# Kernel tuning notes

Measured on AMD Instinct MI355X. Metric: run time of the kernel, lower is better.

The kernel has to match this reference:

```python
import jax, jax.numpy as jnp
import numpy as np

N_NODES = 100000
N_EDGES = 1600000
D = 64


def setup_inputs() -> dict:
    key = jax.random.key(0)
    ks = jax.random.split(key, 8)
    x = jax.random.normal(ks[0], (N_NODES, D), dtype=jnp.float32)
    edge_index = jax.random.randint(ks[1], (2, N_EDGES), 0, N_NODES, dtype=jnp.int64)
    scale = 1.0 / np.sqrt(D)
    W1 = jax.random.normal(ks[2], (D, D), dtype=jnp.float32) * scale
    W2 = jax.random.normal(ks[3], (D, D), dtype=jnp.float32) * scale
    W3 = jax.random.normal(ks[4], (D, D), dtype=jnp.float32) * scale
    b1 = jnp.zeros((D,), dtype=jnp.float32)
    b2 = jnp.zeros((D,), dtype=jnp.float32)
    b3 = jnp.zeros((D,), dtype=jnp.float32)
    return {"x": x, "edge_index": edge_index, "W1": W1, "b1": b1,
            "W2": W2, "b2": b2, "W3": W3, "b3": b3}


def reference(x, edge_index, W1, b1, W2, b2, W3, b3):
    # 3-layer GCN (PyG GCNConv semantics): add self-loops, symmetric
    # degree normalization, linear transform, scatter-add aggregation.
    # Dropout is identity at inference.
    N = x.shape[0]
    loops = jnp.arange(N, dtype=edge_index.dtype)
    src = jnp.concatenate([edge_index[0], loops])  # [E+N]
    dst = jnp.concatenate([edge_index[1], loops])  # [E+N]
    # degree of each node (in-degree at dst, self-loops included)
    deg = jax.ops.segment_sum(jnp.ones(src.shape[0], dtype=x.dtype), dst,
                              num_segments=N)
    dis = jnp.where(deg > 0, jax.lax.rsqrt(jnp.maximum(deg, 1.0)), 0.0)
    norm = dis[src] * dis[dst]  # [E+N]

    def gcn_layer(h, W, b):
        h = h @ W                                   # [N, d_out]
        msg = norm[:, None] * h[src]                # gather + scale, [E+N, d_out]
        agg = jax.ops.segment_sum(msg, dst, num_segments=N)  # scatter-add
        return agg + b

    h = jax.nn.relu(gcn_layer(x, W1, b1))
    h = jax.nn.relu(gcn_layer(h, W2, b2))
    return gcn_layer(h, W3, b3)
```

## Files before the change

kernel.cpp:

```cpp
#include <hip/hip_runtime.h>

#define NN 100000
#define NE 1600000

typedef __attribute__((ext_vector_type(16))) int i32x16;

#define NBKT 196
#define NBLK 128
#define EPB  (NE / NBLK)
#define PTH  512

__global__ __launch_bounds__(PTH) void k_pcount(const int* __restrict__ dst,
                                                int* __restrict__ pcount) {
  __shared__ int lcnt[NBKT];
  int t = threadIdx.x, b = blockIdx.x;
  for (int i = t; i < NBKT; i += PTH) lcnt[i] = 0;
  __syncthreads();
  int base = b * EPB;
  for (int i = t; i < EPB; i += PTH)
    atomicAdd(&lcnt[dst[base + i] >> 9], 1);
  __syncthreads();
  for (int i = t; i < NBKT; i += PTH)
    pcount[i * NBLK + b] = lcnt[i];
}

__global__ __launch_bounds__(1024) void k_pscan(int* __restrict__ pcount) {
  __shared__ int sh[1024];
  const int TOT = NBKT * NBLK;
  int t = threadIdx.x;
  int base = t * 25;
  int v[25];
  int s = 0;
  #pragma unroll
  for (int k = 0; k < 25; ++k) {
    v[k] = (base + k < TOT) ? pcount[base + k] : 0;
    s += v[k];
  }
  sh[t] = s;
  __syncthreads();
  for (int off = 1; off < 1024; off <<= 1) {
    int x = (t >= off) ? sh[t - off] : 0;
    __syncthreads();
    sh[t] += x;
    __syncthreads();
  }
  int ex = sh[t] - s;
  #pragma unroll
  for (int k = 0; k < 25; ++k) {
    if (base + k < TOT) pcount[base + k] = ex;
    ex += v[k];
  }
}

__global__ __launch_bounds__(PTH) void k_pscatter(const int* __restrict__ src,
                                                  const int* __restrict__ dst,
                                                  const int* __restrict__ pcount,
                                                  int* __restrict__ staged) {
  __shared__ int lpos[NBKT];
  int t = threadIdx.x, b = blockIdx.x;
  for (int i = t; i < NBKT; i += PTH) lpos[i] = pcount[i * NBLK + b];
  __syncthreads();
  int base = b * EPB;
  for (int i = t; i < EPB; i += PTH) {
    int s = src[base + i], d = dst[base + i];
    int pos = atomicAdd(&lpos[d >> 9], 1);
    staged[pos] = s | ((d & 511) << 17);
  }
}

__global__ __launch_bounds__(PTH) void k_bucket(const int* __restrict__ staged,
                                                const int* __restrict__ pcount,
                                                int* __restrict__ rowptr,
                                                float* __restrict__ dis,
                                                int* __restrict__ col) {
  __shared__ int lcnt[PTH];
  __shared__ int lscan[PTH];
  __shared__ int lpos[PTH];
  int t = threadIdx.x, bkt = blockIdx.x;
  int sbeg = pcount[bkt * NBLK];
  int send = (bkt == NBKT - 1) ? NE : pcount[(bkt + 1) * NBLK];

  lcnt[t] = 0;
  __syncthreads();
  for (int i = sbeg + t; i < send; i += PTH)
    atomicAdd(&lcnt[(unsigned)staged[i] >> 17], 1);
  __syncthreads();

  int v = lcnt[t];
  lscan[t] = v;
  __syncthreads();
  for (int off = 1; off < PTH; off <<= 1) {
    int x = (t >= off) ? lscan[t - off] : 0;
    __syncthreads();
    lscan[t] += x;
    __syncthreads();
  }
  int gbase = sbeg + lscan[t] - v;
  int node = bkt * 512 + t;
  if (node < NN) {
    rowptr[node] = gbase;
    dis[node] = rsqrtf((float)(v + 1));
  }
  lpos[t] = gbase;
  if (bkt == NBKT - 1 && t == 0) rowptr[NN] = NE;
  __syncthreads();

  for (int i = sbeg + t; i < send; i += PTH) {
    int e = staged[i];
    col[atomicAdd(&lpos[(unsigned)e >> 17], 1)] = e & 0x1FFFF;
  }
}

__device__ __forceinline__ unsigned bf16rne(float x) {
  unsigned u = __float_as_uint(x);
  return (u + 0x7fffu + ((u >> 16) & 1u)) >> 16;
}

__global__ __launch_bounds__(256) void k_xform(const float* __restrict__ h,
                                               const float* __restrict__ W,
                                               const float* __restrict__ dis,
                                               unsigned short* __restrict__ ts) {
  __shared__ float hT[64][132];
  __shared__ float Wl[64][68];
  const int tid = threadIdx.x;
  const int R0 = blockIdx.x * 128;

  {
    const float4* W4 = (const float4*)W;
    #pragma unroll
    for (int j = 0; j < 4; ++j) {
      int idx = tid + 256 * j;
      float4 v = W4[idx];
      int k = idx >> 4;
      int c = (idx & 15) * 4;
      Wl[k][c + 0] = v.x; Wl[k][c + 1] = v.y;
      Wl[k][c + 2] = v.z; Wl[k][c + 3] = v.w;
    }
  }
  {
    #pragma unroll
    for (int j = 0; j < 8; ++j) {
      int idx = tid + 256 * j;
      int r = idx >> 4;
      int k = (idx & 15) * 4;
      int rg = R0 + r; if (rg > NN - 1) rg = NN - 1;
      float4 v = *(const float4*)(h + (size_t)rg * 64 + k);
      hT[k + 0][r] = v.x; hT[k + 1][r] = v.y;
      hT[k + 2][r] = v.z; hT[k + 3][r] = v.w;
    }
  }
  __syncthreads();

  const int tx = tid & 7;
  const int ty = tid >> 3;
  float acc[4][8];
  #pragma unroll
  for (int i = 0; i < 4; ++i)
    #pragma unroll
    for (int j = 0; j < 8; ++j) acc[i][j] = 0.f;

  #pragma unroll 4
  for (int k = 0; k < 64; ++k) {
    float4 hv = *(const float4*)&hT[k][ty * 4];
    float4 w0 = *(const float4*)&Wl[k][tx * 8];
    float4 w1 = *(const float4*)&Wl[k][tx * 8 + 4];
    float hh[4] = {hv.x, hv.y, hv.z, hv.w};
    float wc[8] = {w0.x, w0.y, w0.z, w0.w, w1.x, w1.y, w1.z, w1.w};
    #pragma unroll
    for (int i = 0; i < 4; ++i)
      #pragma unroll
      for (int j = 0; j < 8; ++j)
        acc[i][j] = fmaf(hh[i], wc[j], acc[i][j]);
  }

  #pragma unroll
  for (int i = 0; i < 4; ++i) {
    int r = R0 + ty * 4 + i;
    if (r < NN) {
      float dr = dis[r];
      uint4 pk;
      pk.x = bf16rne(acc[i][0] * dr) | (bf16rne(acc[i][1] * dr) << 16);
      pk.y = bf16rne(acc[i][2] * dr) | (bf16rne(acc[i][3] * dr) << 16);
      pk.z = bf16rne(acc[i][4] * dr) | (bf16rne(acc[i][5] * dr) << 16);
      pk.w = bf16rne(acc[i][6] * dr) | (bf16rne(acc[i][7] * dr) << 16);
      *(uint4*)(ts + (size_t)r * 64 + tx * 8) = pk;
    }
  }
}

__global__ __launch_bounds__(256) void k_fuse(
    const unsigned short* __restrict__ ts, const int* __restrict__ rowptr,
    const int* __restrict__ col, const float* __restrict__ dis,
    const float* __restrict__ bias, const float* __restrict__ Wn,
    unsigned short* __restrict__ tnext)
{
  __shared__ float Wl[64][68];
  __shared__ float hh[32][68];
  const int tid  = threadIdx.x;
  const int lane = tid & 63;
  const int slot = lane >> 4;
  const int fq   = lane & 15;
  const int R0   = blockIdx.x * 32;
  const int wloc = tid >> 6;
  const int wid  = __builtin_amdgcn_readfirstlane(
                     (int)(blockIdx.x * 4 + wloc));
  const int n0   = wid * 8;

  {
    const float4* W4 = (const float4*)Wn;
    #pragma unroll
    for (int j = 0; j < 4; ++j) {
      int idx = tid + 256 * j;
      float4 v = W4[idx];
      int k = idx >> 4;
      int c = (idx & 15) * 4;
      Wl[k][c + 0] = v.x; Wl[k][c + 1] = v.y;
      Wl[k][c + 2] = v.z; Wl[k][c + 3] = v.w;
    }
  }

  const float4 bv = *(const float4*)(bias + fq * 4);
  const float m_self = (slot == 0) ? 1.f : 0.f;

  i32x16 rp;
  asm volatile("s_load_dwordx16 %0, %1, 0x0\n\ts_waitcnt lgkmcnt(0)"
               : "=s"(rp) : "s"(rowptr + n0));

  float a[8][4];
  #pragma unroll
  for (int i = 0; i < 8; ++i) {
    const uint2 sv = *(const uint2*)(ts + (size_t)(n0 + i) * 64 + fq * 4);
    a[i][0] = m_self * __uint_as_float(sv.x << 16);
    a[i][1] = m_self * __uint_as_float(sv.x & 0xffff0000u);
    a[i][2] = m_self * __uint_as_float(sv.y << 16);
    a[i][3] = m_self * __uint_as_float(sv.y & 0xffff0000u);
  }

  #pragma unroll
  for (int i = 0; i < 8; ++i) {
    const int r0 = rp[i], r1 = rp[i + 1];
    #pragma unroll
    for (int s = 0; s < 4; ++s) {
      int e = r0 + s * 4 + slot;
      int c = col[e];
      bool valid = e < r1;
      c = valid ? c : 0;
      float m = valid ? 1.f : 0.f;
      const uint2 gv = *(const uint2*)(ts + (size_t)c * 64 + fq * 4);
      a[i][0] = fmaf(m, __uint_as_float(gv.x << 16),         a[i][0]);
      a[i][1] = fmaf(m, __uint_as_float(gv.x & 0xffff0000u), a[i][1]);
      a[i][2] = fmaf(m, __uint_as_float(gv.y << 16),         a[i][2]);
      a[i][3] = fmaf(m, __uint_as_float(gv.y & 0xffff0000u), a[i][3]);
    }
  }

  #pragma unroll
  for (int i = 0; i < 8; ++i) {
    const int r1 = rp[i + 1];
    #pragma unroll 1
    for (int e0 = rp[i] + 16; e0 < r1; e0 += 8) {
      #pragma unroll
      for (int s = 0; s < 2; ++s) {
        int e = e0 + s * 4 + slot;
        int c = col[e];
        bool valid = e < r1;
        c = valid ? c : 0;
        float m = valid ? 1.f : 0.f;
        const uint2 gv = *(const uint2*)(ts + (size_t)c * 64 + fq * 4);
        a[i][0] = fmaf(m, __uint_as_float(gv.x << 16),         a[i][0]);
        a[i][1] = fmaf(m, __uint_as_float(gv.x & 0xffff0000u), a[i][1]);
        a[i][2] = fmaf(m, __uint_as_float(gv.y << 16),         a[i][2]);
        a[i][3] = fmaf(m, __uint_as_float(gv.y & 0xffff0000u), a[i][3]);
      }
    }
  }

  #pragma unroll
  for (int i = 0; i < 8; ++i) {
    const int node = n0 + i;
    const float dn = dis[node];
    float s0 = a[i][0], s1 = a[i][1], s2 = a[i][2], s3 = a[i][3];
    s0 += __shfl_xor(s0, 16); s1 += __shfl_xor(s1, 16);
    s2 += __shfl_xor(s2, 16); s3 += __shfl_xor(s3, 16);
    s0 += __shfl_xor(s0, 32); s1 += __shfl_xor(s1, 32);
    s2 += __shfl_xor(s2, 32); s3 += __shfl_xor(s3, 32);
    float4 o;
    o.x = fmaxf(fmaf(dn, s0, bv.x), 0.f);
    o.y = fmaxf(fmaf(dn, s1, bv.y), 0.f);
    o.z = fmaxf(fmaf(dn, s2, bv.z), 0.f);
    o.w = fmaxf(fmaf(dn, s3, bv.w), 0.f);
    if (lane < 16)
      *(float4*)&hh[wloc * 8 + i][fq * 4] = o;
  }
  __syncthreads();

  const int tx = tid & 7;
  const int ty = tid >> 3;
  float acc[8];
  #pragma unroll
  for (int j = 0; j < 8; ++j) acc[j] = 0.f;
  #pragma unroll 4
  for (int k = 0; k < 64; ++k) {
    float hkv = hh[ty][k];
    float4 w0 = *(const float4*)&Wl[k][tx * 8];
    float4 w1 = *(const float4*)&Wl[k][tx * 8 + 4];
    acc[0] = fmaf(hkv, w0.x, acc[0]); acc[1] = fmaf(hkv, w0.y, acc[1]);
    acc[2] = fmaf(hkv, w0.z, acc[2]); acc[3] = fmaf(hkv, w0.w, acc[3]);
    acc[4] = fmaf(hkv, w1.x, acc[4]); acc[5] = fmaf(hkv, w1.y, acc[5]);
    acc[6] = fmaf(hkv, w1.z, acc[6]); acc[7] = fmaf(hkv, w1.w, acc[7]);
  }
  {
    int r = R0 + ty;
    float dr = dis[r];
    uint4 pk;
    pk.x = bf16rne(acc[0] * dr) | (bf16rne(acc[1] * dr) << 16);
    pk.y = bf16rne(acc[2] * dr) | (bf16rne(acc[3] * dr) << 16);
    pk.z = bf16rne(acc[4] * dr) | (bf16rne(acc[5] * dr) << 16);
    pk.w = bf16rne(acc[6] * dr) | (bf16rne(acc[7] * dr) << 16);
    *(uint4*)(tnext + (size_t)r * 64 + tx * 8) = pk;
  }
}

__global__ __launch_bounds__(256) void k_agg(
    const unsigned short* __restrict__ ts, const int* __restrict__ rowptr,
    const int* __restrict__ col, const float* __restrict__ dis,
    const float* __restrict__ bias, float* __restrict__ out)
{
  const int lane = threadIdx.x & 63;
  const int slot = lane >> 4;
  const int fq   = lane & 15;
  const int wid  = __builtin_amdgcn_readfirstlane(
                     (int)((blockIdx.x * blockDim.x + threadIdx.x) >> 6));
  const int n0   = wid * 8;
  if (n0 >= NN) return;

  const float4 bv = *(const float4*)(bias + fq * 4);
  const float m_self = (slot == 0) ? 1.f : 0.f;

  i32x16 rp;
  asm volatile("s_load_dwordx16 %0, %1, 0x0\n\ts_waitcnt lgkmcnt(0)"
               : "=s"(rp) : "s"(rowptr + n0));

  float a[8][4];
  #pragma unroll
  for (int i = 0; i < 8; ++i) {
    const uint2 sv = *(const uint2*)(ts + (size_t)(n0 + i) * 64 + fq * 4);
    a[i][0] = m_self * __uint_as_float(sv.x << 16);
    a[i][1] = m_self * __uint_as_float(sv.x & 0xffff0000u);
    a[i][2] = m_self * __uint_as_float(sv.y << 16);
    a[i][3] = m_self * __uint_as_float(sv.y & 0xffff0000u);
  }

  #pragma unroll
  for (int i = 0; i < 8; ++i) {
    const int r0 = rp[i], r1 = rp[i + 1];
    #pragma unroll
    for (int s = 0; s < 4; ++s) {
      int e = r0 + s * 4 + slot;
      int c = col[e];
      bool valid = e < r1;
      c = valid ? c : 0;
      float m = valid ? 1.f : 0.f;
      const uint2 gv = *(const uint2*)(ts + (size_t)c * 64 + fq * 4);
      a[i][0] = fmaf(m, __uint_as_float(gv.x << 16),         a[i][0]);
      a[i][1] = fmaf(m, __uint_as_float(gv.x & 0xffff0000u), a[i][1]);
      a[i][2] = fmaf(m, __uint_as_float(gv.y << 16),         a[i][2]);
      a[i][3] = fmaf(m, __uint_as_float(gv.y & 0xffff0000u), a[i][3]);
    }
  }

  #pragma unroll
  for (int i = 0; i < 8; ++i) {
    const int r1 = rp[i + 1];
    #pragma unroll 1
    for (int e0 = rp[i] + 16; e0 < r1; e0 += 8) {
      #pragma unroll
      for (int s = 0; s < 2; ++s) {
        int e = e0 + s * 4 + slot;
        int c = col[e];
        bool valid = e < r1;
        c = valid ? c : 0;
        float m = valid ? 1.f : 0.f;
        const uint2 gv = *(const uint2*)(ts + (size_t)c * 64 + fq * 4);
        a[i][0] = fmaf(m, __uint_as_float(gv.x << 16),         a[i][0]);
        a[i][1] = fmaf(m, __uint_as_float(gv.x & 0xffff0000u), a[i][1]);
        a[i][2] = fmaf(m, __uint_as_float(gv.y << 16),         a[i][2]);
        a[i][3] = fmaf(m, __uint_as_float(gv.y & 0xffff0000u), a[i][3]);
      }
    }
  }

  #pragma unroll
  for (int i = 0; i < 8; ++i) {
    const int node = n0 + i;
    const float dn = dis[node];
    float s0 = a[i][0], s1 = a[i][1], s2 = a[i][2], s3 = a[i][3];
    s0 += __shfl_xor(s0, 16); s1 += __shfl_xor(s1, 16);
    s2 += __shfl_xor(s2, 16); s3 += __shfl_xor(s3, 16);
    s0 += __shfl_xor(s0, 32); s1 += __shfl_xor(s1, 32);
    s2 += __shfl_xor(s2, 32); s3 += __shfl_xor(s3, 32);
    float4 o;
    o.x = fmaf(dn, s0, bv.x); o.y = fmaf(dn, s1, bv.y);
    o.z = fmaf(dn, s2, bv.z); o.w = fmaf(dn, s3, bv.w);
    if (lane < 16)
      *(float4*)(out + (size_t)node * 64 + fq * 4) = o;
  }
}

extern "C" void kernel_launch(void* const* d_in, const int* in_sizes, int n_in,
                              void* d_out, int out_size, void* d_ws, size_t ws_size,
                              hipStream_t stream) {
  const float* x  = (const float*)d_in[0];
  const int*   ei = (const int*)d_in[1];
  const float* W1 = (const float*)d_in[2];
  const float* b1 = (const float*)d_in[3];
  const float* W2 = (const float*)d_in[4];
  const float* b2 = (const float*)d_in[5];
  const float* W3 = (const float*)d_in[6];
  const float* b3 = (const float*)d_in[7];
  float* out = (float*)d_out;

  const int* src = ei;
  const int* dst = ei + NE;

  char* ws = (char*)d_ws;
  size_t off = 0;
  auto alloc = [&](size_t bytes) {
    void* p = ws + off;
    off = (off + bytes + 255) & ~(size_t)255;
    return p;
  };
  int*   pcount = (int*)alloc((size_t)NBKT * NBLK * 4);
  int*   rowptr = (int*)alloc((size_t)(NN + 1 + 16) * 4);
  float* dis    = (float*)alloc((size_t)NN * 4);
  int*   staged = (int*)alloc((size_t)NE * 4);
  int*   col    = (int*)alloc((size_t)(NE + 64) * 4);
  unsigned short* tb1 =
      (unsigned short*)alloc((size_t)NN * 64 * 2);
  unsigned short* tb2 =
      (unsigned short*)alloc((size_t)NN * 64 * 2);
  (void)ws_size; (void)in_sizes; (void)n_in; (void)out_size;

  k_pcount  <<<NBLK, PTH, 0, stream>>>(dst, pcount);
  k_pscan   <<<1, 1024, 0, stream>>>(pcount);
  k_pscatter<<<NBLK, PTH, 0, stream>>>(src, dst, pcount, staged);
  k_bucket  <<<NBKT, PTH, 0, stream>>>(staged, pcount, rowptr, dis, col);

  const int XF_BLOCKS = (NN + 127) / 128;
  const int FB        = NN / 32;

  k_xform<<<XF_BLOCKS, 256, 0, stream>>>(x, W1, dis, tb1);
  k_fuse <<<FB, 256, 0, stream>>>(tb1, rowptr, col, dis, b1, W2, tb2);
  k_fuse <<<FB, 256, 0, stream>>>(tb2, rowptr, col, dis, b2, W3, tb1);
  k_agg  <<<FB, 256, 0, stream>>>(tb1, rowptr, col, dis, b3, out);
}
```

Baseline: 203.7 us.

## Split-K the fused 32x64x64 GEMM across waves with register tiling and LDS reduction

```diff
diff --git a/kernel.cpp b/kernel.cpp
--- a/kernel.cpp
+++ b/kernel.cpp
@@ -194,8 +194,11 @@
     const float* __restrict__ bias, const float* __restrict__ Wn,
     unsigned short* __restrict__ tnext)
 {
-  __shared__ float Wl[64][68];
-  __shared__ float hh[32][68];
+  __shared__ __align__(16) char smem[27648];
+  float (*Wl)[68] = reinterpret_cast<float(*)[68]>(smem);
+  float (*hT)[40] = reinterpret_cast<float(*)[40]>(smem + 17408);
+  float (*red)[65] = reinterpret_cast<float(*)[65]>(smem);
+
   const int tid  = threadIdx.x;
   const int lane = tid & 63;
   const int slot = lane >> 4;
@@ -284,40 +287,68 @@
     s2 += __shfl_xor(s2, 16); s3 += __shfl_xor(s3, 16);
     s0 += __shfl_xor(s0, 32); s1 += __shfl_xor(s1, 32);
     s2 += __shfl_xor(s2, 32); s3 += __shfl_xor(s3, 32);
-    float4 o;
-    o.x = fmaxf(fmaf(dn, s0, bv.x), 0.f);
-    o.y = fmaxf(fmaf(dn, s1, bv.y), 0.f);
-    o.z = fmaxf(fmaf(dn, s2, bv.z), 0.f);
-    o.w = fmaxf(fmaf(dn, s3, bv.w), 0.f);
-    if (lane < 16)
-      *(float4*)&hh[wloc * 8 + i][fq * 4] = o;
-  }
-  __syncthreads();
-
-  const int tx = tid & 7;
-  const int ty = tid >> 3;
-  float acc[8];
-  #pragma unroll
-  for (int j = 0; j < 8; ++j) acc[j] = 0.f;
-  #pragma unroll 4
-  for (int k = 0; k < 64; ++k) {
-    float hkv = hh[ty][k];
-    float4 w0 = *(const float4*)&Wl[k][tx * 8];
-    float4 w1 = *(const float4*)&Wl[k][tx * 8 + 4];
-    acc[0] = fmaf(hkv, w0.x, acc[0]); acc[1] = fmaf(hkv, w0.y, acc[1]);
-    acc[2] = fmaf(hkv, w0.z, acc[2]); acc[3] = fmaf(hkv, w0.w, acc[3]);
-    acc[4] = fmaf(hkv, w1.x, acc[4]); acc[5] = fmaf(hkv, w1.y, acc[5]);
-    acc[6] = fmaf(hkv, w1.z, acc[6]); acc[7] = fmaf(hkv, w1.w, acc[7]);
-  }
-  {
-    int r = R0 + ty;
-    float dr = dis[r];
-    uint4 pk;
-    pk.x = bf16rne(acc[0] * dr) | (bf16rne(acc[1] * dr) << 16);
-    pk.y = bf16rne(acc[2] * dr) | (bf16rne(acc[3] * dr) << 16);
-    pk.z = bf16rne(acc[4] * dr) | (bf16rne(acc[5] * dr) << 16);
-    pk.w = bf16rne(acc[6] * dr) | (bf16rne(acc[7] * dr) << 16);
-    *(uint4*)(tnext + (size_t)r * 64 + tx * 8) = pk;
+    if (lane < 16) {
+      const int row = wloc * 8 + i;
+      hT[fq * 4 + 0][row] = fmaxf(fmaf(dn, s0, bv.x), 0.f);
+      hT[fq * 4 + 1][row] = fmaxf(fmaf(dn, s1, bv.y), 0.f);
+      hT[fq * 4 + 2][row] = fmaxf(fmaf(dn, s2, bv.z), 0.f);
+      hT[fq * 4 + 3][row] = fmaxf(fmaf(dn, s3, bv.w), 0.f);
+    }
+  }
+  __syncthreads();
+
+  const int kg = wloc;
+  const int cg = lane & 7;
+  const int rg = lane >> 3;
+  float acc[4][8];
+  #pragma unroll
+  for (int i = 0; i < 4; ++i)
+    #pragma unroll
+    for (int j = 0; j < 8; ++j) acc[i][j] = 0.f;
+
+  #pragma unroll
+  for (int kk = 0; kk < 16; ++kk) {
+    const int k = kg * 16 + kk;
+    float4 hv = *(const float4*)&hT[k][rg * 4];
+    float4 w0 = *(const float4*)&Wl[k][cg * 8];
+    float4 w1 = *(const float4*)&Wl[k][cg * 8 + 4];
+    float hh4[4] = {hv.x, hv.y, hv.z, hv.w};
+    float wc[8] = {w0.x, w0.y, w0.z, w0.w, w1.x, w1.y, w1.z, w1.w};
+    #pragma unroll
+    for (int i = 0; i < 4; ++i)
+      #pragma unroll
+      for (int j = 0; j < 8; ++j)
+        acc[i][j] = fmaf(hh4[i], wc[j], acc[i][j]);
+  }
+  __syncthreads();
+
+  if (kg > 0) {
+    #pragma unroll
+    for (int i = 0; i < 4; ++i)
+      #pragma unroll
+      for (int j = 0; j < 8; ++j)
+        red[(kg - 1) * 32 + i * 8 + j][lane] = acc[i][j];
+  }
+  __syncthreads();
+  if (kg == 0) {
+    #pragma unroll
+    for (int g = 0; g < 3; ++g)
+      #pragma unroll
+      for (int i = 0; i < 4; ++i)
+        #pragma unroll
+        for (int j = 0; j < 8; ++j)
+          acc[i][j] += red[g * 32 + i * 8 + j][lane];
+    #pragma unroll
+    for (int i = 0; i < 4; ++i) {
+      const int r = R0 + rg * 4 + i;
+      const float dr = dis[r];
+      uint4 pk;
+      pk.x = bf16rne(acc[i][0] * dr) | (bf16rne(acc[i][1] * dr) << 16);
+      pk.y = bf16rne(acc[i][2] * dr) | (bf16rne(acc[i][3] * dr) << 16);
+      pk.z = bf16rne(acc[i][4] * dr) | (bf16rne(acc[i][5] * dr) << 16);
+      pk.w = bf16rne(acc[i][6] * dr) | (bf16rne(acc[i][7] * dr) << 16);
+      *(uint4*)(tnext + (size_t)r * 64 + cg * 8) = pk;
+    }
   }
 }
 
```

After: 242.7 us. 19.1% more time.
